# Performance work log

Hardware: AMD Instinct MI355X
Metric: run time of the kernel (lower is better)

Reference implementation:

```python
import jax, jax.numpy as jnp
import numpy as np

DIM = 1024
N_HEADS = 16
D_HEAD = DIM // N_HEADS


def setup_inputs() -> dict:
    key = jax.random.key(0)
    ks = jax.random.split(key, 7)
    s = DIM ** -0.5
    return {
        "x": jax.random.normal(ks[0], (4, 2048, DIM), dtype=jnp.float32),
        "Wq": jax.random.normal(ks[1], (DIM, DIM), dtype=jnp.float32) * s,
        "bq": jax.random.normal(ks[2], (DIM,), dtype=jnp.float32) * 0.02,
        "Wk": jax.random.normal(ks[3], (DIM, DIM), dtype=jnp.float32) * s,
        "bk": jax.random.normal(ks[4], (DIM,), dtype=jnp.float32) * 0.02,
        "Wv": jax.random.normal(ks[5], (DIM, DIM), dtype=jnp.float32) * s,
        "bv": jax.random.normal(ks[6], (DIM,), dtype=jnp.float32) * 0.02,
    }


def reference(x, Wq, bq, Wk, bk, Wv, bv):
    B, N, D = x.shape
    H, Dh = N_HEADS, D_HEAD

    def split_heads(t):
        # b n (h d) -> b h n d
        return t.reshape(B, N, H, Dh).transpose(0, 2, 1, 3)

    q = split_heads(x @ Wq + bq)
    k = split_heads(x @ Wk + bk)
    v = split_heads(x @ Wv + bv)

    scale = Dh ** -0.5
    logit = jnp.einsum("bhnd,bhmd->bhnm", q, k) * scale  # [B,H,N,N]
    attn = jax.nn.softmax(logit, axis=-1)
    out = jnp.einsum("bhnm,bhmd->bhnd", attn, v)
    # b h n d -> b n (h d)
    return out.transpose(0, 2, 1, 3).reshape(B, N, D)
```

## Files before the change

### kernel.cpp

```cpp
#include <hip/hip_runtime.h>
#include <hip/hip_bf16.h>
#include <stdint.h>

#define BB 4
#define SEQ 2048
#define DIM 1024
#define NH 16
#define DH 64
#define MM (BB*SEQ)

typedef unsigned short u16;
typedef __attribute__((ext_vector_type(8))) __bf16 bf16x8;
typedef __attribute__((ext_vector_type(4))) float floatx4;
typedef __attribute__((ext_vector_type(16))) float floatx16;
typedef __attribute__((ext_vector_type(2))) float floatx2;
typedef __attribute__((ext_vector_type(4))) unsigned short u16x4;
typedef __attribute__((ext_vector_type(2))) unsigned int uint2v;

#define QSCALE 0.18033688011112042f

__device__ __forceinline__ u16 f2bf(float f) {
    union { float f; unsigned u; } v; v.f = f;
    unsigned u = v.u;
    u += 0x7FFF + ((u >> 16) & 1);
    return (u16)(u >> 16);
}

__device__ __forceinline__ bf16x8 ldb8(const u16* p) {
    return *(const bf16x8*)(const void*)p;
}

__device__ __forceinline__ void async_copy16(const u16* g, u16* l) {
    __builtin_amdgcn_global_load_lds(
        (const __attribute__((address_space(1))) unsigned int*)g,
        (__attribute__((address_space(3))) unsigned int*)l, 16, 0, 0);
}

__device__ __forceinline__ floatx16 mfma32(bf16x8 a, bf16x8 b, floatx16 c) {
    return __builtin_amdgcn_mfma_f32_32x32x16_bf16(a, b, c, 0, 0, 0);
}

__device__ __forceinline__ unsigned cvtpk(float lo, float hi) {
    unsigned r;
    asm("v_cvt_pk_bf16_f32 %0, %1, %2" : "=v"(r) : "v"(lo), "v"(hi));
    return r;
}

__global__ __launch_bounds__(256)
void prep(const float* __restrict__ x, u16* __restrict__ xb,
          const float* __restrict__ Wq, const float* __restrict__ Wk,
          const float* __restrict__ Wv, u16* __restrict__ Wt) {
    const int bx = blockIdx.x;
    const int tid = threadIdx.x;
    if (bx < 8192) {
        const size_t i = ((size_t)bx * 256 + tid) * 4;
        float4 f = *(const float4*)(x + i);
        u16x4 o = { f2bf(f.x), f2bf(f.y), f2bf(f.z), f2bf(f.w) };
        *(u16x4*)(xb + i) = o;
        return;
    }
    const int idx = bx - 8192;
    const int t = idx >> 8;
    const int r2 = idx & 255;
    const int k0 = (r2 >> 4) * 64, n0 = (r2 & 15) * 64;
    const float* W = (t == 0) ? Wq : (t == 1) ? Wk : Wv;
    u16* D = Wt + (size_t)t * DIM * DIM;
    __shared__ u16 T[64][65];
    #pragma unroll
    for (int p = 0; p < 4; p++) {
        const int r = p * 16 + (tid >> 4), c = (tid & 15) * 4;
        float4 f = *(const float4*)(W + (size_t)(k0 + r) * DIM + n0 + c);
        T[c + 0][r] = f2bf(f.x); T[c + 1][r] = f2bf(f.y);
        T[c + 2][r] = f2bf(f.z); T[c + 3][r] = f2bf(f.w);
    }
    __syncthreads();
    #pragma unroll
    for (int p = 0; p < 4; p++) {
        const int rn = p * 16 + (tid >> 4), ck = (tid & 15) * 4;
        u16x4 v = { T[rn][ck], T[rn][ck + 1], T[rn][ck + 2], T[rn][ck + 3] };
        *(u16x4*)(D + (size_t)(n0 + rn) * DIM + k0 + ck) = v;
    }
}

__global__ __launch_bounds__(256, 3)
void qkv_gemm3(const u16* __restrict__ xb, const u16* __restrict__ Wt,
               const float* __restrict__ bq, const float* __restrict__ bk,
               const float* __restrict__ bv, u16* __restrict__ ws) {
    __shared__ u16 As[2][4096];
    __shared__ u16 Bs[2][4096];

    const int m0 = blockIdx.x * 128;
    const int t  = blockIdx.y >> 3;
    const int c0 = (blockIdx.y & 7) * 128;
    const u16* Wtb = Wt + (size_t)t * DIM * DIM;
    const float* bias = (t == 0) ? bq : (t == 1) ? bk : bv;
    const float osc = (t == 0) ? QSCALE : 1.0f;
    u16* dst = ws + (size_t)t * ((size_t)MM * DIM);

    const int tid  = threadIdx.x;
    const int lane = tid & 63;
    const int w    = tid >> 6;
    const int wr = w >> 1, wc = w & 1;
    const int g = lane >> 4, ln = lane & 15;

    floatx4 acc[4][4];
    #pragma unroll
    for (int i = 0; i < 4; i++)
        #pragma unroll
        for (int j = 0; j < 4; j++) acc[i][j] = (floatx4){0.f,0.f,0.f,0.f};

    const int srow = w*16 + (lane >> 2);
    const int gseg = (lane & 3) ^ ((lane >> 3) & 3);
    const u16* gA = xb  + (size_t)(m0 + srow) * DIM + gseg*8;
    const u16* gB = Wtb + (size_t)(c0 + srow) * DIM + gseg*8;

    async_copy16(gA,                   &As[0][w*512]);
    async_copy16(gA + (size_t)64*DIM,  &As[0][2048 + w*512]);
    async_copy16(gB,                   &Bs[0][w*512]);
    async_copy16(gB + (size_t)64*DIM,  &Bs[0][2048 + w*512]);
    __syncthreads();

    const int xu = (ln >> 1) & 3;

    for (int it = 0; it < 32; it++) {
        const int cur = it & 1;
        if (it < 31) {
            const int nxt = cur ^ 1;
            const int kk = (it + 1) * 32;
            async_copy16(gA + kk,                  &As[nxt][w*512]);
            async_copy16(gA + kk + (size_t)64*DIM, &As[nxt][2048 + w*512]);
            async_copy16(gB + kk,                  &Bs[nxt][w*512]);
            async_copy16(gB + kk + (size_t)64*DIM, &Bs[nxt][2048 + w*512]);
        }

        bf16x8 a[4], b[4];
        #pragma unroll
        for (int fr = 0; fr < 4; fr++)
            a[fr] = ldb8(&As[cur][(wr*64 + fr*16 + ln)*32 + (g ^ xu)*8]);
        #pragma unroll
        for (int fc = 0; fc < 4; fc++)
            b[fc] = ldb8(&Bs[cur][(wc*64 + fc*16 + ln)*32 + (g ^ xu)*8]);

        if (t < 2) {
            #pragma unroll
            for (int fr = 0; fr < 4; fr++)
                #pragma unroll
                for (int fc = 0; fc < 4; fc++)
                    acc[fr][fc] = __builtin_amdgcn_mfma_f32_16x16x32_bf16(
                        b[fc], a[fr], acc[fr][fc], 0, 0, 0);
        } else {
            #pragma unroll
            for (int fr = 0; fr < 4; fr++)
                #pragma unroll
                for (int fc = 0; fc < 4; fc++)
                    acc[fr][fc] = __builtin_amdgcn_mfma_f32_16x16x32_bf16(
                        a[fr], b[fc], acc[fr][fc], 0, 0, 0);
        }
        __syncthreads();
    }

    if (t < 2) {
        #pragma unroll
        for (int fc = 0; fc < 4; fc++) {
            const int cc = c0 + wc*64 + fc*16 + g*4;
            const float4 b4 = *(const float4*)&bias[cc];
            const int h = cc >> 6, d = cc & 63;
            #pragma unroll
            for (int fr = 0; fr < 4; fr++) {
                const int tok = m0 + wr*64 + fr*16 + ln;
                const int bidx = tok >> 11, nn = tok & 2047;
                u16x4 v = { f2bf((acc[fr][fc][0] + b4.x) * osc),
                            f2bf((acc[fr][fc][1] + b4.y) * osc),
                            f2bf((acc[fr][fc][2] + b4.z) * osc),
                            f2bf((acc[fr][fc][3] + b4.w) * osc) };
                *(u16x4*)&dst[((size_t)(bidx*NH + h)*SEQ + nn)*DH + d] = v;
            }
        }
    } else {
        #pragma unroll
        for (int fc = 0; fc < 4; fc++) {
            const int cc = c0 + wc*64 + fc*16 + ln;
            const float bias_v = bias[cc];
            const int h = cc >> 6, d = cc & 63;
            #pragma unroll
            for (int fr = 0; fr < 4; fr++) {
                const int mrow = m0 + wr*64 + fr*16 + g*4;
                const int bidx = mrow >> 11, nn = mrow & 2047;
                u16x4 v = { f2bf(acc[fr][fc][0] + bias_v), f2bf(acc[fr][fc][1] + bias_v),
                            f2bf(acc[fr][fc][2] + bias_v), f2bf(acc[fr][fc][3] + bias_v) };
                *(u16x4*)&dst[((size_t)(bidx*NH + h)*DH + d)*SEQ + nn] = v;
            }
        }
    }
}

#define LDA 40
__global__ __launch_bounds__(256)
void qkv_gemm(const float* __restrict__ x,
              const float* __restrict__ Wq, const float* __restrict__ bq,
              const float* __restrict__ Wk, const float* __restrict__ bk,
              const float* __restrict__ Wv, const float* __restrict__ bv,
              u16* __restrict__ ws) {
    __shared__ u16 As[128 * LDA];
    __shared__ u16 Bs[128 * LDA];
    const int m0 = blockIdx.x * 128;
    const int t  = blockIdx.y >> 3;
    const int c0 = (blockIdx.y & 7) * 128;
    const float* W    = (t == 0) ? Wq : (t == 1) ? Wk : Wv;
    const float* bias = (t == 0) ? bq : (t == 1) ? bk : bv;
    const float osc = (t == 0) ? QSCALE : 1.0f;
    u16* dst = ws + (size_t)t * ((size_t)MM * DIM);
    const int tid  = threadIdx.x;
    const int lane = tid & 63;
    const int wave = tid >> 6;
    const int wr = wave >> 1, wc = wave & 1;
    const int g = lane >> 4, ln = lane & 15;
    floatx4 acc[4][4];
    #pragma unroll
    for (int i = 0; i < 4; i++)
        #pragma unroll
        for (int j = 0; j < 4; j++) acc[i][j] = (floatx4){0.f,0.f,0.f,0.f};
    const int ar  = tid >> 1;
    const int ak  = (tid & 1) * 16;
    const int bkr = tid & 31;
    const int bc  = (tid >> 5) * 16;
    for (int kk = 0; kk < DIM; kk += 32) {
        {
            const float4* s4 = (const float4*)(x + (size_t)(m0 + ar) * DIM + kk + ak);
            float4 f0 = s4[0], f1 = s4[1], f2 = s4[2], f3 = s4[3];
            unsigned pk[8];
            pk[0] = f2bf(f0.x) | ((unsigned)f2bf(f0.y) << 16);
            pk[1] = f2bf(f0.z) | ((unsigned)f2bf(f0.w) << 16);
            pk[2] = f2bf(f1.x) | ((unsigned)f2bf(f1.y) << 16);
            pk[3] = f2bf(f1.z) | ((unsigned)f2bf(f1.w) << 16);
            pk[4] = f2bf(f2.x) | ((unsigned)f2bf(f2.y) << 16);
            pk[5] = f2bf(f2.z) | ((unsigned)f2bf(f2.w) << 16);
            pk[6] = f2bf(f3.x) | ((unsigned)f2bf(f3.y) << 16);
            pk[7] = f2bf(f3.z) | ((unsigned)f2bf(f3.w) << 16);
            uint4* d = (uint4*)&As[ar * LDA + ak];
            d[0] = make_uint4(pk[0], pk[1], pk[2], pk[3]);
            d[1] = make_uint4(pk[4], pk[5], pk[6], pk[7]);
        }
        {
            const float4* s4 = (const float4*)(W + (size_t)(kk + bkr) * DIM + c0 + bc);
            float4 f0 = s4[0], f1 = s4[1], f2 = s4[2], f3 = s4[3];
            float fv[16] = {f0.x,f0.y,f0.z,f0.w, f1.x,f1.y,f1.z,f1.w,
                            f2.x,f2.y,f2.z,f2.w, f3.x,f3.y,f3.z,f3.w};
            #pragma unroll
            for (int j = 0; j < 16; j++)
                Bs[(bc + j) * LDA + bkr] = f2bf(fv[j]);
        }
        __syncthreads();
        bf16x8 a[4], b[4];
        #pragma unroll
        for (int fr = 0; fr < 4; fr++)
            a[fr] = ldb8(&As[(wr*64 + fr*16 + ln) * LDA + g*8]);
        #pragma unroll
        for (int fc = 0; fc < 4; fc++)
            b[fc] = ldb8(&Bs[(wc*64 + fc*16 + ln) * LDA + g*8]);
        #pragma unroll
        for (int fr = 0; fr < 4; fr++)
            #pragma unroll
            for (int fc = 0; fc < 4; fc++)
                acc[fr][fc] = __builtin_amdgcn_mfma_f32_16x16x32_bf16(
                    a[fr], b[fc], acc[fr][fc], 0, 0, 0);
        __syncthreads();
    }
    #pragma unroll
    for (int fc = 0; fc < 4; fc++) {
        const int cc = c0 + wc*64 + fc*16 + ln;
        const float bias_v = bias[cc];
        const int h = cc >> 6, d = cc & 63;
        #pragma unroll
        for (int fr = 0; fr < 4; fr++) {
            #pragma unroll
            for (int rr = 0; rr < 4; rr++) {
                const int mrow = m0 + wr*64 + fr*16 + g*4 + rr;
                const int bidx = mrow >> 11, nn = mrow & 2047;
                const float val = (acc[fr][fc][rr] + bias_v) * osc;
                size_t idx;
                if (t < 2) idx = ((size_t)(bidx*NH + h)*SEQ + nn)*DH + d;
                else       idx = ((size_t)(bidx*NH + h)*DH + d)*SEQ + nn;
                dst[idx] = f2bf(val);
            }
        }
    }
}

__global__ __launch_bounds__(512, 4)
void attn10(const u16* __restrict__ ws, float* __restrict__ out) {
    const int bid = blockIdx.x;
    const int qt = bid >> 6;
    const int bh = bid & 63;
    const int b  = bh >> 4;
    const int h  = bh & 15;

    const u16* Qw = ws;
    const u16* Kw = ws + (size_t)MM * DIM;
    const u16* Vt = ws + 2 * (size_t)MM * DIM;

    __shared__ u16 Kbuf[4][4096];
    __shared__ u16 Vbuf[4][4096];

    const int tid  = threadIdx.x;
    const int lane = tid & 63;
    const int w    = tid >> 6;
    const int l31  = lane & 31;
    const int hi   = lane >> 5;
    const int c7   = lane & 7;
    const int q0w  = qt*256 + w*32;

    const int srow = w*8 + (lane >> 3);
    const int sseg = (lane & 7) ^ ((lane >> 3) & 7);
    const u16* kg = Kw + ((size_t)bh*SEQ + srow)*DH + sseg*8;
    const u16* vg = Vt + ((size_t)bh*DH + srow)*SEQ + sseg*8;

    bf16x8 qf[4];
    {
        const u16* qp = Qw + ((size_t)bh*SEQ + q0w + l31)*DH + hi*8;
        #pragma unroll
        for (int ds = 0; ds < 4; ds++) qf[ds] = ldb8(qp + ds*16);
    }

    floatx16 accO[2];
    #pragma unroll
    for (int fd = 0; fd < 2; fd++)
        #pragma unroll
        for (int r = 0; r < 16; r++) accO[fd][r] = 0.f;
    floatx2 lr2 = (floatx2){0.f, 0.f};
    floatx16 fz;
    #pragma unroll
    for (int r = 0; r < 16; r++) fz[r] = 0.f;

    #pragma unroll
    for (int t = 0; t < 3; t++) {
        async_copy16(kg + (size_t)t*64*DH, &Kbuf[t][w*512]);
        async_copy16(vg + (size_t)t*64,    &Vbuf[t][w*512]);
    }

    for (int kt = 0; kt < 32; kt++) {
        if (kt < 30)      asm volatile("s_waitcnt vmcnt(4)" ::: "memory");
        else if (kt == 30) asm volatile("s_waitcnt vmcnt(2)" ::: "memory");
        else               asm volatile("s_waitcnt vmcnt(0)" ::: "memory");
        __builtin_amdgcn_s_barrier();
        __builtin_amdgcn_sched_barrier(0);

        if (kt < 29) {
            const int t3 = kt + 3;
            async_copy16(kg + (size_t)t3*64*DH, &Kbuf[t3 & 3][w*512]);
            async_copy16(vg + (size_t)t3*64,    &Vbuf[t3 & 3][w*512]);
        }

        const u16* Kc = &Kbuf[kt & 3][0];
        const u16* Vc = &Vbuf[kt & 3][0];

        #pragma unroll
        for (int kb = 0; kb < 2; kb++) {
            const u16* krow = &Kc[(kb*32 + l31)*64];
            bf16x8 kf0 = ldb8(&krow[((0 + hi) ^ c7)*8]);
            bf16x8 kf1 = ldb8(&krow[((2 + hi) ^ c7)*8]);
            bf16x8 kf2 = ldb8(&krow[((4 + hi) ^ c7)*8]);
            bf16x8 kf3 = ldb8(&krow[((6 + hi) ^ c7)*8]);
            floatx16 z = mfma32(kf0, qf[0], fz);
            z = mfma32(kf1, qf[1], z);
            z = mfma32(kf2, qf[2], z);
            z = mfma32(kf3, qf[3], z);

            float p[16];
            #pragma unroll
            for (int r = 0; r < 16; r++) p[r] = __builtin_amdgcn_exp2f(z[r]);
            #pragma unroll
            for (int i = 0; i < 8; i++)
                lr2 += (floatx2){p[2*i], p[2*i+1]};
            unsigned c[8];
            #pragma unroll
            for (int i = 0; i < 8; i++) c[i] = cvtpk(p[2*i], p[2*i+1]);

            uint2v s02 = __builtin_amdgcn_permlane32_swap(c[0], c[2], false, false);
            uint2v s13 = __builtin_amdgcn_permlane32_swap(c[1], c[3], false, false);
            uint2v s46 = __builtin_amdgcn_permlane32_swap(c[4], c[6], false, false);
            uint2v s57 = __builtin_amdgcn_permlane32_swap(c[5], c[7], false, false);
            union { unsigned u[4]; bf16x8 v; } bp0, bp1;
            bp0.u[0] = s02[0]; bp0.u[1] = s13[0]; bp0.u[2] = s02[1]; bp0.u[3] = s13[1];
            bp1.u[0] = s46[0]; bp1.u[1] = s57[0]; bp1.u[2] = s46[1]; bp1.u[3] = s57[1];

            bf16x8 av00 = ldb8(&Vc[(0*32 + l31)*64 + ((kb*4 + 0 + hi) ^ c7)*8]);
            bf16x8 av01 = ldb8(&Vc[(0*32 + l31)*64 + ((kb*4 + 2 + hi) ^ c7)*8]);
            bf16x8 av10 = ldb8(&Vc[(1*32 + l31)*64 + ((kb*4 + 0 + hi) ^ c7)*8]);
            bf16x8 av11 = ldb8(&Vc[(1*32 + l31)*64 + ((kb*4 + 2 + hi) ^ c7)*8]);
            accO[0] = mfma32(av00, bp0.v, accO[0]);
            accO[1] = mfma32(av10, bp0.v, accO[1]);
            accO[0] = mfma32(av01, bp1.v, accO[0]);
            accO[1] = mfma32(av11, bp1.v, accO[1]);
        }
    }

    {
        float v = lr2[0] + lr2[1];
        v += __shfl_xor(v, 32, 64);
        const float inv = 1.0f / v;
        const int n = q0w + l31;
        float* orow = &out[((size_t)b*SEQ + n)*DIM + h*DH];
        #pragma unroll
        for (int fd = 0; fd < 2; fd++)
            #pragma unroll
            for (int rp = 0; rp < 4; rp++) {
                const int d = fd*32 + rp*8 + hi*4;
                float4 o = { accO[fd][rp*4+0]*inv, accO[fd][rp*4+1]*inv,
                             accO[fd][rp*4+2]*inv, accO[fd][rp*4+3]*inv };
                *(float4*)&orow[d] = o;
            }
    }
}

extern "C" void kernel_launch(void* const* d_in, const int* in_sizes, int n_in,
                              void* d_out, int out_size, void* d_ws, size_t ws_size,
                              hipStream_t stream) {
    const float* x  = (const float*)d_in[0];
    const float* Wq = (const float*)d_in[1];
    const float* bq = (const float*)d_in[2];
    const float* Wk = (const float*)d_in[3];
    const float* bk = (const float*)d_in[4];
    const float* Wv = (const float*)d_in[5];
    const float* bv = (const float*)d_in[6];
    u16* ws = (u16*)d_ws;
    float* out = (float*)d_out;

    const size_t need = (size_t)4 * MM * DIM * 2 + (size_t)3 * DIM * DIM * 2;
    if (ws_size >= need) {
        u16* xb = ws + (size_t)3 * MM * DIM;
        u16* Wt = ws + (size_t)4 * MM * DIM;
        prep<<<dim3(8192 + 768), 256, 0, stream>>>(x, xb, Wq, Wk, Wv, Wt);
        qkv_gemm3<<<dim3(MM/128, 24), 256, 0, stream>>>(xb, Wt, bq, bk, bv, ws);
    } else {
        qkv_gemm<<<dim3(MM/128, 24), 256, 0, stream>>>(x, Wq, bq, Wk, bk, Wv, bv, ws);
    }
    attn10<<<dim3((SEQ/256) * NH * BB), 512, 0, stream>>>(ws, out);
}
```

Before: 255.6 us.

## Deepen QKV GEMM prefetch pipeline to four LDS stages with vmcnt waits

Replaces the double-buffered QKV GEMM main loop with a four-stage LDS ring that prefetches three K-tiles ahead. Explicit s_waitcnt vmcnt counts plus a single barrier per iteration replace the full __syncthreads at the end of each step. This is meant to hide global-to-LDS latency better and cut barrier overhead. The cost is double the shared memory and a lower launch-bounds occupancy target (2 blocks instead of 3), and correctness depends on the async copies being counted by vmcnt as assumed.

```diff
diff --git a/kernel.cpp b/kernel.cpp
--- a/kernel.cpp
+++ b/kernel.cpp
@@ -82,12 +82,12 @@
     }
 }
 
-__global__ __launch_bounds__(256, 3)
-void qkv_gemm3(const u16* __restrict__ xb, const u16* __restrict__ Wt,
+__global__ __launch_bounds__(256, 2)
+void qkv_gemm4(const u16* __restrict__ xb, const u16* __restrict__ Wt,
                const float* __restrict__ bq, const float* __restrict__ bk,
                const float* __restrict__ bv, u16* __restrict__ ws) {
-    __shared__ u16 As[2][4096];
-    __shared__ u16 Bs[2][4096];
+    __shared__ u16 As[4][4096];
+    __shared__ u16 Bs[4][4096];
 
     const int m0 = blockIdx.x * 128;
     const int t  = blockIdx.y >> 3;
@@ -114,32 +114,45 @@
     const u16* gA = xb  + (size_t)(m0 + srow) * DIM + gseg*8;
     const u16* gB = Wtb + (size_t)(c0 + srow) * DIM + gseg*8;
 
-    async_copy16(gA,                   &As[0][w*512]);
-    async_copy16(gA + (size_t)64*DIM,  &As[0][2048 + w*512]);
-    async_copy16(gB,                   &Bs[0][w*512]);
-    async_copy16(gB + (size_t)64*DIM,  &Bs[0][2048 + w*512]);
-    __syncthreads();
+    #pragma unroll
+    for (int pt = 0; pt < 3; pt++) {
+        const int kk = pt * 32;
+        async_copy16(gA + kk,                  &As[pt][w*512]);
+        async_copy16(gA + kk + (size_t)64*DIM, &As[pt][2048 + w*512]);
+        async_copy16(gB + kk,                  &Bs[pt][w*512]);
+        async_copy16(gB + kk + (size_t)64*DIM, &Bs[pt][2048 + w*512]);
+    }
 
     const int xu = (ln >> 1) & 3;
 
     for (int it = 0; it < 32; it++) {
-        const int cur = it & 1;
-        if (it < 31) {
-            const int nxt = cur ^ 1;
-            const int kk = (it + 1) * 32;
-            async_copy16(gA + kk,                  &As[nxt][w*512]);
-            async_copy16(gA + kk + (size_t)64*DIM, &As[nxt][2048 + w*512]);
-            async_copy16(gB + kk,                  &Bs[nxt][w*512]);
-            async_copy16(gB + kk + (size_t)64*DIM, &Bs[nxt][2048 + w*512]);
-        }
+        if (it < 30)       asm volatile("s_waitcnt vmcnt(8)" ::: "memory");
+        else if (it == 30) asm volatile("s_waitcnt vmcnt(4)" ::: "memory");
+        else               asm volatile("s_waitcnt vmcnt(0)" ::: "memory");
+        __builtin_amdgcn_s_barrier();
+        __builtin_amdgcn_sched_barrier(0);
+
+        if (it < 29) {
+            const int t3 = it + 3;
+            const int kk = t3 * 32;
+            u16* a3 = &As[t3 & 3][0];
+            u16* b3 = &Bs[t3 & 3][0];
+            async_copy16(gA + kk,                  a3 + w*512);
+            async_copy16(gA + kk + (size_t)64*DIM, a3 + 2048 + w*512);
+            async_copy16(gB + kk,                  b3 + w*512);
+            async_copy16(gB + kk + (size_t)64*DIM, b3 + 2048 + w*512);
+        }
+
+        const u16* Ac = &As[it & 3][0];
+        const u16* Bc = &Bs[it & 3][0];
 
         bf16x8 a[4], b[4];
         #pragma unroll
         for (int fr = 0; fr < 4; fr++)
-            a[fr] = ldb8(&As[cur][(wr*64 + fr*16 + ln)*32 + (g ^ xu)*8]);
+            a[fr] = ldb8(&Ac[(wr*64 + fr*16 + ln)*32 + (g ^ xu)*8]);
         #pragma unroll
         for (int fc = 0; fc < 4; fc++)
-            b[fc] = ldb8(&Bs[cur][(wc*64 + fc*16 + ln)*32 + (g ^ xu)*8]);
+            b[fc] = ldb8(&Bc[(wc*64 + fc*16 + ln)*32 + (g ^ xu)*8]);
 
         if (t < 2) {
             #pragma unroll
@@ -156,7 +169,6 @@
                     acc[fr][fc] = __builtin_amdgcn_mfma_f32_16x16x32_bf16(
                         a[fr], b[fc], acc[fr][fc], 0, 0, 0);
         }
-        __syncthreads();
     }
 
     if (t < 2) {
@@ -431,7 +443,7 @@
         u16* xb = ws + (size_t)3 * MM * DIM;
         u16* Wt = ws + (size_t)4 * MM * DIM;
         prep<<<dim3(8192 + 768), 256, 0, stream>>>(x, xb, Wq, Wk, Wv, Wt);
-        qkv_gemm3<<<dim3(MM/128, 24), 256, 0, stream>>>(xb, Wt, bq, bk, bv, ws);
+        qkv_gemm4<<<dim3(MM/128, 24), 256, 0, stream>>>(xb, Wt, bq, bk, bv, ws);
     } else {
         qkv_gemm<<<dim3(MM/128, 24), 256, 0, stream>>>(x, Wq, bq, Wk, bk, Wv, bv, ws);
     }
```

Result: slower. 261.0 us (+2.1%).

## Process two 32-row query tiles per wave to reuse K/V fragments

Applied to the files above, without the earlier changes.

The attention kernel now runs 4 waves of 256 threads instead of 8, and each wave handles 64 query rows as two 32-row sub-tiles. Each K and V fragment read from shared memory feeds two MFMAs, halving LDS reads per FLOP. Each thread issues twice as many async copies, and the vmcnt waits are doubled to match. The cost is roughly double the accumulator and Q registers per wave, and fewer waves resident per CU to hide latency.

```diff
diff --git a/kernel.cpp b/kernel.cpp
--- a/kernel.cpp
+++ b/kernel.cpp
@@ -287,8 +287,8 @@
     }
 }
 
-__global__ __launch_bounds__(512, 4)
-void attn10(const u16* __restrict__ ws, float* __restrict__ out) {
+__global__ __launch_bounds__(256, 2)
+void attn11(const u16* __restrict__ ws, float* __restrict__ out) {
     const int bid = blockIdx.x;
     const int qt = bid >> 6;
     const int bh = bid & 63;
@@ -308,47 +308,54 @@
     const int l31  = lane & 31;
     const int hi   = lane >> 5;
     const int c7   = lane & 7;
-    const int q0w  = qt*256 + w*32;
-
-    const int srow = w*8 + (lane >> 3);
+    const int q0w  = qt*256 + w*64;
+
+    const int srow = w*16 + (lane >> 3);
     const int sseg = (lane & 7) ^ ((lane >> 3) & 7);
     const u16* kg = Kw + ((size_t)bh*SEQ + srow)*DH + sseg*8;
     const u16* vg = Vt + ((size_t)bh*DH + srow)*SEQ + sseg*8;
 
-    bf16x8 qf[4];
-    {
-        const u16* qp = Qw + ((size_t)bh*SEQ + q0w + l31)*DH + hi*8;
-        #pragma unroll
-        for (int ds = 0; ds < 4; ds++) qf[ds] = ldb8(qp + ds*16);
-    }
-
-    floatx16 accO[2];
-    #pragma unroll
-    for (int fd = 0; fd < 2; fd++)
-        #pragma unroll
-        for (int r = 0; r < 16; r++) accO[fd][r] = 0.f;
-    floatx2 lr2 = (floatx2){0.f, 0.f};
+    bf16x8 qf[2][4];
+    #pragma unroll
+    for (int qs = 0; qs < 2; qs++) {
+        const u16* qp = Qw + ((size_t)bh*SEQ + q0w + qs*32 + l31)*DH + hi*8;
+        #pragma unroll
+        for (int ds = 0; ds < 4; ds++) qf[qs][ds] = ldb8(qp + ds*16);
+    }
+
+    floatx16 accO[2][2];
+    #pragma unroll
+    for (int qs = 0; qs < 2; qs++)
+        #pragma unroll
+        for (int fd = 0; fd < 2; fd++)
+            #pragma unroll
+            for (int r = 0; r < 16; r++) accO[qs][fd][r] = 0.f;
+    floatx2 lr2[2] = { (floatx2){0.f,0.f}, (floatx2){0.f,0.f} };
     floatx16 fz;
     #pragma unroll
     for (int r = 0; r < 16; r++) fz[r] = 0.f;
 
     #pragma unroll
     for (int t = 0; t < 3; t++) {
-        async_copy16(kg + (size_t)t*64*DH, &Kbuf[t][w*512]);
-        async_copy16(vg + (size_t)t*64,    &Vbuf[t][w*512]);
+        async_copy16(kg + (size_t)t*64*DH,           &Kbuf[t][w*1024]);
+        async_copy16(kg + (size_t)t*64*DH + 8*DH,    &Kbuf[t][w*1024 + 512]);
+        async_copy16(vg + (size_t)t*64,              &Vbuf[t][w*1024]);
+        async_copy16(vg + (size_t)t*64 + (size_t)8*SEQ, &Vbuf[t][w*1024 + 512]);
     }
 
     for (int kt = 0; kt < 32; kt++) {
-        if (kt < 30)      asm volatile("s_waitcnt vmcnt(4)" ::: "memory");
-        else if (kt == 30) asm volatile("s_waitcnt vmcnt(2)" ::: "memory");
+        if (kt < 30)       asm volatile("s_waitcnt vmcnt(8)" ::: "memory");
+        else if (kt == 30) asm volatile("s_waitcnt vmcnt(4)" ::: "memory");
         else               asm volatile("s_waitcnt vmcnt(0)" ::: "memory");
         __builtin_amdgcn_s_barrier();
         __builtin_amdgcn_sched_barrier(0);
 
         if (kt < 29) {
             const int t3 = kt + 3;
-            async_copy16(kg + (size_t)t3*64*DH, &Kbuf[t3 & 3][w*512]);
-            async_copy16(vg + (size_t)t3*64,    &Vbuf[t3 & 3][w*512]);
+            async_copy16(kg + (size_t)t3*64*DH,           &Kbuf[t3 & 3][w*1024]);
+            async_copy16(kg + (size_t)t3*64*DH + 8*DH,    &Kbuf[t3 & 3][w*1024 + 512]);
+            async_copy16(vg + (size_t)t3*64,              &Vbuf[t3 & 3][w*1024]);
+            async_copy16(vg + (size_t)t3*64 + (size_t)8*SEQ, &Vbuf[t3 & 3][w*1024 + 512]);
         }
 
         const u16* Kc = &Kbuf[kt & 3][0];
@@ -361,53 +368,79 @@
             bf16x8 kf1 = ldb8(&krow[((2 + hi) ^ c7)*8]);
             bf16x8 kf2 = ldb8(&krow[((4 + hi) ^ c7)*8]);
             bf16x8 kf3 = ldb8(&krow[((6 + hi) ^ c7)*8]);
-            floatx16 z = mfma32(kf0, qf[0], fz);
-            z = mfma32(kf1, qf[1], z);
-            z = mfma32(kf2, qf[2], z);
-            z = mfma32(kf3, qf[3], z);
-
-            float p[16];
-            #pragma unroll
-            for (int r = 0; r < 16; r++) p[r] = __builtin_amdgcn_exp2f(z[r]);
-            #pragma unroll
-            for (int i = 0; i < 8; i++)
-                lr2 += (floatx2){p[2*i], p[2*i+1]};
-            unsigned c[8];
-            #pragma unroll
-            for (int i = 0; i < 8; i++) c[i] = cvtpk(p[2*i], p[2*i+1]);
-
-            uint2v s02 = __builtin_amdgcn_permlane32_swap(c[0], c[2], false, false);
-            uint2v s13 = __builtin_amdgcn_permlane32_swap(c[1], c[3], false, false);
-            uint2v s46 = __builtin_amdgcn_permlane32_swap(c[4], c[6], false, false);
-            uint2v s57 = __builtin_amdgcn_permlane32_swap(c[5], c[7], false, false);
-            union { unsigned u[4]; bf16x8 v; } bp0, bp1;
-            bp0.u[0] = s02[0]; bp0.u[1] = s13[0]; bp0.u[2] = s02[1]; bp0.u[3] = s13[1];
-            bp1.u[0] = s46[0]; bp1.u[1] = s57[0]; bp1.u[2] = s46[1]; bp1.u[3] = s57[1];
+
+            floatx16 z0 = mfma32(kf0, qf[0][0], fz);
+            floatx16 z1 = mfma32(kf0, qf[1][0], fz);
+            z0 = mfma32(kf1, qf[0][1], z0);
+            z1 = mfma32(kf1, qf[1][1], z1);
+            z0 = mfma32(kf2, qf[0][2], z0);
+            z1 = mfma32(kf2, qf[1][2], z1);
+            z0 = mfma32(kf3, qf[0][3], z0);
+            z1 = mfma32(kf3, qf[1][3], z1);
+
+            union { unsigned u[4]; bf16x8 v; } bpA0, bpA1, bpB0, bpB1;
+            {
+                float p[16];
+                #pragma unroll
+                for (int r = 0; r < 16; r++) p[r] = __builtin_amdgcn_exp2f(z0[r]);
+                #pragma unroll
+                for (int i = 0; i < 8; i++) lr2[0] += (floatx2){p[2*i], p[2*i+1]};
+                unsigned c[8];
+                #pragma unroll
+                for (int i = 0; i < 8; i++) c[i] = cvtpk(p[2*i], p[2*i+1]);
+                uint2v s02 = __builtin_amdgcn_permlane32_swap(c[0], c[2], false, false);
+                uint2v s13 = __builtin_amdgcn_permlane32_swap(c[1], c[3], false, false);
+                uint2v s46 = __builtin_amdgcn_permlane32_swap(c[4], c[6], false, false);
+                uint2v s57 = __builtin_amdgcn_permlane32_swap(c[5], c[7], false, false);
+                bpA0.u[0] = s02[0]; bpA0.u[1] = s13[0]; bpA0.u[2] = s02[1]; bpA0.u[3] = s13[1];
+                bpA1.u[0] = s46[0]; bpA1.u[1] = s57[0]; bpA1.u[2] = s46[1]; bpA1.u[3] = s57[1];
+            }
+            {
+                float p[16];
+                #pragma unroll
+                for (int r = 0; r < 16; r++) p[r] = __builtin_amdgcn_exp2f(z1[r]);
+                #pragma unroll
+                for (int i = 0; i < 8; i++) lr2[1] += (floatx2){p[2*i], p[2*i+1]};
+                unsigned c[8];
+                #pragma unroll
+                for (int i = 0; i < 8; i++) c[i] = cvtpk(p[2*i], p[2*i+1]);
+                uint2v s02 = __builtin_amdgcn_permlane32_swap(c[0], c[2], false, false);
+                uint2v s13 = __builtin_amdgcn_permlane32_swap(c[1], c[3], false, false);
+                uint2v s46 = __builtin_amdgcn_permlane32_swap(c[4], c[6], false, false);
+                uint2v s57 = __builtin_amdgcn_permlane32_swap(c[5], c[7], false, false);
+                bpB0.u[0] = s02[0]; bpB0.u[1] = s13[0]; bpB0.u[2] = s02[1]; bpB0.u[3] = s13[1];
+                bpB1.u[0] = s46[0]; bpB1.u[1] = s57[0]; bpB1.u[2] = s46[1]; bpB1.u[3] = s57[1];
+            }
 
             bf16x8 av00 = ldb8(&Vc[(0*32 + l31)*64 + ((kb*4 + 0 + hi) ^ c7)*8]);
             bf16x8 av01 = ldb8(&Vc[(0*32 + l31)*64 + ((kb*4 + 2 + hi) ^ c7)*8]);
             bf16x8 av10 = ldb8(&Vc[(1*32 + l31)*64 + ((kb*4 + 0 + hi) ^ c7)*8]);
             bf16x8 av11 = ldb8(&Vc[(1*32 + l31)*64 + ((kb*4 + 2 + hi) ^ c7)*8]);
-            accO[0] = mfma32(av00, bp0.v, accO[0]);
-            accO[1] = mfma32(av10, bp0.v, accO[1]);
-            accO[0] = mfma32(av01, bp1.v, accO[0]);
-            accO[1] = mfma32(av11, bp1.v, accO[1]);
-        }
-    }
-
-    {
-        float v = lr2[0] + lr2[1];
+            accO[0][0] = mfma32(av00, bpA0.v, accO[0][0]);
+            accO[1][0] = mfma32(av00, bpB0.v, accO[1][0]);
+            accO[0][1] = mfma32(av10, bpA0.v, accO[0][1]);
+            accO[1][1] = mfma32(av10, bpB0.v, accO[1][1]);
+            accO[0][0] = mfma32(av01, bpA1.v, accO[0][0]);
+            accO[1][0] = mfma32(av01, bpB1.v, accO[1][0]);
+            accO[0][1] = mfma32(av11, bpA1.v, accO[0][1]);
+            accO[1][1] = mfma32(av11, bpB1.v, accO[1][1]);
+        }
+    }
+
+    #pragma unroll
+    for (int qs = 0; qs < 2; qs++) {
+        float v = lr2[qs][0] + lr2[qs][1];
         v += __shfl_xor(v, 32, 64);
         const float inv = 1.0f / v;
-        const int n = q0w + l31;
+        const int n = q0w + qs*32 + l31;
         float* orow = &out[((size_t)b*SEQ + n)*DIM + h*DH];
         #pragma unroll
         for (int fd = 0; fd < 2; fd++)
             #pragma unroll
             for (int rp = 0; rp < 4; rp++) {
                 const int d = fd*32 + rp*8 + hi*4;
-                float4 o = { accO[fd][rp*4+0]*inv, accO[fd][rp*4+1]*inv,
-                             accO[fd][rp*4+2]*inv, accO[fd][rp*4+3]*inv };
+                float4 o = { accO[qs][fd][rp*4+0]*inv, accO[qs][fd][rp*4+1]*inv,
+                             accO[qs][fd][rp*4+2]*inv, accO[qs][fd][rp*4+3]*inv };
                 *(float4*)&orow[d] = o;
             }
     }
@@ -435,5 +468,5 @@
     } else {
         qkv_gemm<<<dim3(MM/128, 24), 256, 0, stream>>>(x, Wq, bq, Wk, bk, Wv, bv, ws);
     }
-    attn10<<<dim3((SEQ/256) * NH * BB), 512, 0, stream>>>(ws, out);
-}
+    attn11<<<dim3((SEQ/256) * NH * BB), 256, 0, stream>>>(ws, out);
+}
```

Result: faster. 250.4 us (-2.0%).
